# Kernel optimization log

Hardware: AMD Instinct MI355X
Metric: run time of the kernel (lower is better)

## Reference

```python
import jax, jax.numpy as jnp
import numpy as np

GRID = 192          # grid_size (scaled up from the module's toy 32)
H = 0.1             # cell_size
VISC = 0.01         # viscosity
DT = 0.01           # config.time_step, passed as forward's dt
GRAV = 9.81


def setup_inputs() -> dict:
    key = jax.random.key(0)
    velocity_field = jax.random.normal(key, (3, GRID, GRID, GRID), dtype=jnp.float32)
    return {"velocity_field": velocity_field}


def _nb_sum(f):
    # 6-neighbor sum on the interior of the last three axes
    return (f[..., 2:, 1:-1, 1:-1] + f[..., :-2, 1:-1, 1:-1]
            + f[..., 1:-1, 2:, 1:-1] + f[..., 1:-1, :-2, 1:-1]
            + f[..., 1:-1, 1:-1, 2:] + f[..., 1:-1, 1:-1, :-2])


def _fluid_step(vel):
    N = GRID
    dt = DT
    # --- add_gravity ---
    vel = vel.at[2].add(-GRAV * dt)
    # --- advect: semi-Lagrangian backtrace + trilinear interpolation ---
    coords = jnp.arange(N, dtype=vel.dtype)
    X, Y, Z = jnp.meshgrid(coords, coords, coords, indexing='ij')
    pos = jnp.stack([X, Y, Z]) - vel * (dt / H)        # [3,N,N,N] backtraced positions
    pos = jnp.clip(pos, 0.0, float(N - 2))
    i0 = jnp.floor(pos).astype(jnp.int32)              # base corner, i1 = i0+1 <= N-1
    w1 = pos - i0.astype(vel.dtype)
    w0 = 1.0 - w1
    ix, iy, iz = i0[0], i0[1], i0[2]
    wx0, wy0, wz0 = w0[0], w0[1], w0[2]
    wx1, wy1, wz1 = w1[0], w1[1], w1[2]

    def g(di, dj, dk):
        return vel[:, ix + di, iy + dj, iz + dk]        # gather -> [3,N,N,N]

    vel = (g(0, 0, 0) * wx0 * wy0 * wz0 + g(0, 0, 1) * wx0 * wy0 * wz1
           + g(0, 1, 0) * wx0 * wy1 * wz0 + g(0, 1, 1) * wx0 * wy1 * wz1
           + g(1, 0, 0) * wx1 * wy0 * wz0 + g(1, 0, 1) * wx1 * wy0 * wz1
           + g(1, 1, 0) * wx1 * wy1 * wz0 + g(1, 1, 1) * wx1 * wy1 * wz1)
    # --- diffuse: 5 Jacobi sweeps on the interior ---
    alpha = VISC * dt / (H * H)
    inv = 1.0 / (1.0 + 6.0 * alpha)
    for _ in range(5):
        interior = (vel[:, 1:-1, 1:-1, 1:-1] + alpha * _nb_sum(vel)) * inv
        vel = vel.at[:, 1:-1, 1:-1, 1:-1].set(interior)
    # --- project: central-difference divergence, 20 Jacobi pressure sweeps, gradient subtract ---
    div = jnp.zeros((N, N, N), vel.dtype)
    div_int = ((vel[0, 2:, 1:-1, 1:-1] - vel[0, :-2, 1:-1, 1:-1])
               + (vel[1, 1:-1, 2:, 1:-1] - vel[1, 1:-1, :-2, 1:-1])
               + (vel[2, 1:-1, 1:-1, 2:] - vel[2, 1:-1, 1:-1, :-2])) / (2.0 * H)
    div = div.at[1:-1, 1:-1, 1:-1].set(div_int)
    p = jnp.zeros_like(div)
    for _ in range(20):
        p = p.at[1:-1, 1:-1, 1:-1].set((div[1:-1, 1:-1, 1:-1] + _nb_sum(p)) / 6.0)
    inv2h = 1.0 / (2.0 * H)
    vel = vel.at[0, 1:-1, 1:-1, 1:-1].add(-(p[2:, 1:-1, 1:-1] - p[:-2, 1:-1, 1:-1]) * inv2h)
    vel = vel.at[1, 1:-1, 1:-1, 1:-1].add(-(p[1:-1, 2:, 1:-1] - p[1:-1, :-2, 1:-1]) * inv2h)
    vel = vel.at[2, 1:-1, 1:-1, 1:-1].add(-(p[1:-1, 1:-1, 2:] - p[1:-1, 1:-1, :-2]) * inv2h)
    return vel


def reference(velocity_field):
    return _fluid_step(velocity_field)
```

## Files before the change

kernel.cpp:

```cpp
#include <hip/hip_runtime.h>


constexpr int   N      = 192;
constexpr int   N2     = N * N;
constexpr int   N3     = N * N * N;
constexpr float GDT    = 9.81f * 0.01f;
constexpr float SCL    = 0.01f / 0.1f;
constexpr float ALPHA  = 0.01f * 0.01f / (0.1f * 0.1f);
constexpr float INVDIF = 1.0f / (1.0f + 6.0f * ALPHA);
constexpr float INV2H  = 1.0f / (2.0f * 0.1f);
constexpr float SIXTH  = 1.0f / 6.0f;

constexpr int NT4 = (N3 / 4) / 256;
constexpr int SLAB = NT4 / 8;

__device__ __forceinline__ int swz(int b) {
    return (b & 7) * SLAB + (b >> 3);
}

__device__ __forceinline__ void decomp(int id, int& i, int& j, int& k0) {
    i = id / N2;
    const int r = id - i * N2;
    j = r / N;
    k0 = r - j * N;
}

__global__ __launch_bounds__(192) void k_advect(const float* __restrict__ vin,
                                                float* __restrict__ vout) {
    const int k   = threadIdx.x;
    const int lin = blockIdx.y * 192 + blockIdx.x;
    const int x   = lin & 7;
    const int q   = lin >> 3;
    const int il  = q % 24;
    const int j   = q / 24;
    const int i   = x * 24 + il;
    const int id  = (i * N + j) * N + k;

    const float vx = vin[id];
    const float vy = vin[id + N3];
    const float vz = vin[id + 2 * N3] - GDT;

    float px = (float)i - vx * SCL;
    float py = (float)j - vy * SCL;
    float pz = (float)k - vz * SCL;
    const float hi = (float)(N - 2);
    px = fminf(fmaxf(px, 0.0f), hi);
    py = fminf(fmaxf(py, 0.0f), hi);
    pz = fminf(fmaxf(pz, 0.0f), hi);

    const int ix = (int)px;
    const int iy = (int)py;
    const int iz = (int)pz;
    const int base = (ix * N + iy) * N + iz;

    float g[3][8];
#pragma unroll
    for (int c = 0; c < 3; ++c) {
        const float* f = vin + c * N3 + base;
        g[c][0] = f[0];      g[c][1] = f[1];
        g[c][2] = f[N];      g[c][3] = f[N + 1];
        g[c][4] = f[N2];     g[c][5] = f[N2 + 1];
        g[c][6] = f[N2 + N]; g[c][7] = f[N2 + N + 1];
    }

    const float wx1 = px - (float)ix, wy1 = py - (float)iy, wz1 = pz - (float)iz;
    const float wx0 = 1.0f - wx1,     wy0 = 1.0f - wy1,     wz0 = 1.0f - wz1;
    const float w000 = wx0 * wy0 * wz0;
    const float w001 = wx0 * wy0 * wz1;
    const float w010 = wx0 * wy1 * wz0;
    const float w011 = wx0 * wy1 * wz1;
    const float w100 = wx1 * wy0 * wz0;
    const float w101 = wx1 * wy0 * wz1;
    const float w110 = wx1 * wy1 * wz0;
    const float w111 = wx1 * wy1 * wz1;

#pragma unroll
    for (int c = 0; c < 3; ++c) {
        float r = g[c][0] * w000 + g[c][1] * w001
                + g[c][2] * w010 + g[c][3] * w011
                + g[c][4] * w100 + g[c][5] * w101
                + g[c][6] * w110 + g[c][7] * w111;
        if (c == 2) r -= GDT;
        vout[c * N3 + id] = r;
    }
}

__global__ __launch_bounds__(256) void k_diffuse4(const float* __restrict__ vin,
                                                  float* __restrict__ vout) {
    const int gtid = swz(blockIdx.x) * 256 + threadIdx.x;
    const int id   = gtid << 2;
    int i, j, k0; decomp(id, i, j, k0);
    const int b = blockIdx.y * N3 + id;

    const float4 c = *(const float4*)(vin + b);
    float4 out = c;
    if (i != 0 && i != N - 1 && j != 0 && j != N - 1) {
        const float4 ip = *(const float4*)(vin + b + N2);
        const float4 im = *(const float4*)(vin + b - N2);
        const float4 jp = *(const float4*)(vin + b + N);
        const float4 jm = *(const float4*)(vin + b - N);
        const float  km = (k0 > 0)     ? vin[b - 1] : 0.0f;
        const float  kp = (k0 < N - 4) ? vin[b + 4] : 0.0f;
        out.x = (c.x + ALPHA * (im.x + ip.x + jm.x + jp.x + km  + c.y)) * INVDIF;
        out.y = (c.y + ALPHA * (im.y + ip.y + jm.y + jp.y + c.x + c.z)) * INVDIF;
        out.z = (c.z + ALPHA * (im.z + ip.z + jm.z + jp.z + c.y + c.w)) * INVDIF;
        out.w = (c.w + ALPHA * (im.w + ip.w + jm.w + jp.w + c.z + kp )) * INVDIF;
        if (k0 == 0)     out.x = c.x;
        if (k0 == N - 4) out.w = c.w;
    }
    *(float4*)(vout + b) = out;
}

__global__ __launch_bounds__(256) void k_div4(const float* __restrict__ v,
                                              float* __restrict__ dv) {
    const int gtid = swz(blockIdx.x) * 256 + threadIdx.x;
    const int id   = gtid << 2;
    int i, j, k0; decomp(id, i, j, k0);

    float4 out = make_float4(0.f, 0.f, 0.f, 0.f);
    if (i != 0 && i != N - 1 && j != 0 && j != N - 1) {
        const float4 xp = *(const float4*)(v + id + N2);
        const float4 xm = *(const float4*)(v + id - N2);
        const float4 yp = *(const float4*)(v + N3 + id + N);
        const float4 ym = *(const float4*)(v + N3 + id - N);
        const float4 z  = *(const float4*)(v + 2 * N3 + id);
        const float  zm = (k0 > 0)     ? v[2 * N3 + id - 1] : 0.0f;
        const float  zp = (k0 < N - 4) ? v[2 * N3 + id + 4] : 0.0f;
        out.x = ((xp.x - xm.x) + (yp.x - ym.x) + (z.y - zm )) * INV2H;
        out.y = ((xp.y - xm.y) + (yp.y - ym.y) + (z.z - z.x)) * INV2H;
        out.z = ((xp.z - xm.z) + (yp.z - ym.z) + (z.w - z.y)) * INV2H;
        out.w = ((xp.w - xm.w) + (yp.w - ym.w) + (zp  - z.z)) * INV2H;
        if (k0 == 0)     out.x = 0.f;
        if (k0 == N - 4) out.w = 0.f;
    }
    *(float4*)(dv + id) = out;
}

__global__ __launch_bounds__(256) void k_p2_4(const float* __restrict__ dv,
                                              float* __restrict__ p) {
    const int gtid = swz(blockIdx.x) * 256 + threadIdx.x;
    const int id   = gtid << 2;
    int i, j, k0; decomp(id, i, j, k0);

    float4 out = make_float4(0.f, 0.f, 0.f, 0.f);
    if (i != 0 && i != N - 1 && j != 0 && j != N - 1) {
        const float4 c  = *(const float4*)(dv + id);
        const float4 ip = *(const float4*)(dv + id + N2);
        const float4 im = *(const float4*)(dv + id - N2);
        const float4 jp = *(const float4*)(dv + id + N);
        const float4 jm = *(const float4*)(dv + id - N);
        const float  km = (k0 > 0)     ? dv[id - 1] : 0.0f;
        const float  kp = (k0 < N - 4) ? dv[id + 4] : 0.0f;
        out.x = (c.x + (im.x + ip.x + jm.x + jp.x + km  + c.y) * SIXTH) * SIXTH;
        out.y = (c.y + (im.y + ip.y + jm.y + jp.y + c.x + c.z) * SIXTH) * SIXTH;
        out.z = (c.z + (im.z + ip.z + jm.z + jp.z + c.y + c.w) * SIXTH) * SIXTH;
        out.w = (c.w + (im.w + ip.w + jm.w + jp.w + c.z + kp ) * SIXTH) * SIXTH;
        if (k0 == 0)     out.x = 0.f;
        if (k0 == N - 4) out.w = 0.f;
    }
    *(float4*)(p + id) = out;
}

__global__ __launch_bounds__(256) void k_jacobi4(const float* __restrict__ pin,
                                                 const float* __restrict__ dv,
                                                 float* __restrict__ pout) {
    const int gtid = swz(blockIdx.x) * 256 + threadIdx.x;
    const int id   = gtid << 2;
    int i, j, k0; decomp(id, i, j, k0);

    float4 out = make_float4(0.f, 0.f, 0.f, 0.f);
    if (i != 0 && i != N - 1 && j != 0 && j != N - 1) {
        const float4 c  = *(const float4*)(pin + id);
        const float4 ip = *(const float4*)(pin + id + N2);
        const float4 im = *(const float4*)(pin + id - N2);
        const float4 jp = *(const float4*)(pin + id + N);
        const float4 jm = *(const float4*)(pin + id - N);
        const float4 d  = *(const float4*)(dv + id);
        const float  km = (k0 > 0)     ? pin[id - 1] : 0.0f;
        const float  kp = (k0 < N - 4) ? pin[id + 4] : 0.0f;
        out.x = (d.x + im.x + ip.x + jm.x + jp.x + km  + c.y) * SIXTH;
        out.y = (d.y + im.y + ip.y + jm.y + jp.y + c.x + c.z) * SIXTH;
        out.z = (d.z + im.z + ip.z + jm.z + jp.z + c.y + c.w) * SIXTH;
        out.w = (d.w + im.w + ip.w + jm.w + jp.w + c.z + kp ) * SIXTH;
        if (k0 == 0)     out.x = 0.f;
        if (k0 == N - 4) out.w = 0.f;
    }
    *(float4*)(pout + id) = out;
}

__global__ __launch_bounds__(256) void k_grad4(float* __restrict__ vel,
                                               const float* __restrict__ p) {
    const int gtid = swz(blockIdx.x) * 256 + threadIdx.x;
    const int id   = gtid << 2;
    int i, j, k0; decomp(id, i, j, k0);
    if (i == 0 || i == N - 1 || j == 0 || j == N - 1) return;

    const float4 xp = *(const float4*)(p + id + N2);
    const float4 xm = *(const float4*)(p + id - N2);
    const float4 yp = *(const float4*)(p + id + N);
    const float4 ym = *(const float4*)(p + id - N);
    const float4 c  = *(const float4*)(p + id);
    const float  pm = (k0 > 0)     ? p[id - 1] : 0.0f;
    const float  pp = (k0 < N - 4) ? p[id + 4] : 0.0f;

    const bool bx = (k0 == 0);
    const bool bw = (k0 == N - 4);

    float4 v0 = *(float4*)(vel + id);
    if (!bx) v0.x -= (xp.x - xm.x) * INV2H;
             v0.y -= (xp.y - xm.y) * INV2H;
             v0.z -= (xp.z - xm.z) * INV2H;
    if (!bw) v0.w -= (xp.w - xm.w) * INV2H;
    *(float4*)(vel + id) = v0;

    float4 v1 = *(float4*)(vel + N3 + id);
    if (!bx) v1.x -= (yp.x - ym.x) * INV2H;
             v1.y -= (yp.y - ym.y) * INV2H;
             v1.z -= (yp.z - ym.z) * INV2H;
    if (!bw) v1.w -= (yp.w - ym.w) * INV2H;
    *(float4*)(vel + N3 + id) = v1;

    float4 v2 = *(float4*)(vel + 2 * N3 + id);
    if (!bx) v2.x -= (c.y - pm ) * INV2H;
             v2.y -= (c.z - c.x) * INV2H;
             v2.z -= (c.w - c.y) * INV2H;
    if (!bw) v2.w -= (pp  - c.z) * INV2H;
    *(float4*)(vel + 2 * N3 + id) = v2;
}

extern "C" void kernel_launch(void* const* d_in, const int* in_sizes, int n_in,
                              void* d_out, int out_size, void* d_ws, size_t ws_size,
                              hipStream_t stream) {
    const float* vin  = (const float*)d_in[0];
    float*       vout = (float*)d_out;
    float*       ws   = (float*)d_ws;

    float* velB = ws;
    float* dv   = ws;
    float* pA   = ws + N3;
    float* pB   = ws + 2 * N3;

    const dim3 blk(N, 1, 1);
    const dim3 grid1(N, N, 1);
    const dim3 blk4(256, 1, 1);
    const dim3 grid4_1(NT4, 1, 1);
    const dim3 grid4_3(NT4, 3, 1);

    k_advect<<<grid1, blk, 0, stream>>>(vin, velB);

    k_diffuse4<<<grid4_3, blk4, 0, stream>>>(velB, vout);
    k_diffuse4<<<grid4_3, blk4, 0, stream>>>(vout, velB);
    k_diffuse4<<<grid4_3, blk4, 0, stream>>>(velB, vout);
    k_diffuse4<<<grid4_3, blk4, 0, stream>>>(vout, velB);
    k_diffuse4<<<grid4_3, blk4, 0, stream>>>(velB, vout);

    k_div4<<<grid4_1, blk4, 0, stream>>>(vout, dv);
    k_p2_4<<<grid4_1, blk4, 0, stream>>>(dv, pA);
    float* pin  = pA;
    float* pout = pB;
    for (int s = 0; s < 18; ++s) {
        k_jacobi4<<<grid4_1, blk4, 0, stream>>>(pin, dv, pout);
        float* t = pin; pin = pout; pout = t;
    }
    k_grad4<<<grid4_1, blk4, 0, stream>>>(vout, pin);
}
```

Measured before the change: 644.6 us.

## Store pressure and divergence in fp16 and stage advect neighbourhood in LDS

```diff
diff --git a/kernel.cpp b/kernel.cpp
--- a/kernel.cpp
+++ b/kernel.cpp
@@ -1,4 +1,5 @@
 #include <hip/hip_runtime.h>
+#include <hip/hip_fp16.h>
 
 
 constexpr int   N      = 192;
@@ -25,8 +26,24 @@
     k0 = r - j * N;
 }
 
+union H4u { ushort4 u; __half h[4]; };
+__device__ __forceinline__ float4 ldh4(const __half* p) {
+    H4u t; t.u = *(const ushort4*)p;
+    return make_float4(__half2float(t.h[0]), __half2float(t.h[1]),
+                       __half2float(t.h[2]), __half2float(t.h[3]));
+}
+__device__ __forceinline__ void sth4(__half* p, float x, float y, float z, float w) {
+    H4u t;
+    t.h[0] = __float2half(x); t.h[1] = __float2half(y);
+    t.h[2] = __float2half(z); t.h[3] = __float2half(w);
+    *(ushort4*)p = t.u;
+}
+__device__ __forceinline__ float ldh(const __half* p) { return __half2float(*p); }
+
 __global__ __launch_bounds__(192) void k_advect(const float* __restrict__ vin,
                                                 float* __restrict__ vout) {
+    __shared__ float s[27 * 192];
+
     const int k   = threadIdx.x;
     const int lin = blockIdx.y * 192 + blockIdx.x;
     const int x   = lin & 7;
@@ -36,9 +53,29 @@
     const int i   = x * 24 + il;
     const int id  = (i * N + j) * N + k;
 
-    const float vx = vin[id];
-    const float vy = vin[id + N3];
-    const float vz = vin[id + 2 * N3] - GDT;
+    {
+        const int rsub = threadIdx.x / 48;
+        const int col  = (threadIdx.x - rsub * 48) * 4;
+#pragma unroll
+        for (int p = 0; p < 7; ++p) {
+            const int r = p * 4 + rsub;
+            if (r < 27) {
+                const int c   = r / 9;
+                const int rem = r - c * 9;
+                const int di  = rem / 3;
+                const int dj  = rem - di * 3;
+                const int gi  = min(max(i + di - 1, 0), N - 1);
+                const int gj  = min(max(j + dj - 1, 0), N - 1);
+                *(float4*)&s[r * 192 + col] =
+                    *(const float4*)&vin[c * N3 + gi * N2 + gj * N + col];
+            }
+        }
+    }
+    __syncthreads();
+
+    const float vx = s[4 * 192 + k];
+    const float vy = s[13 * 192 + k];
+    const float vz = s[22 * 192 + k] - GDT;
 
     float px = (float)i - vx * SCL;
     float py = (float)j - vy * SCL;
@@ -51,16 +88,33 @@
     const int ix = (int)px;
     const int iy = (int)py;
     const int iz = (int)pz;
-    const int base = (ix * N + iy) * N + iz;
 
     float g[3][8];
+    const bool in = (ix >= i - 1) & (ix <= i) & (iy >= j - 1) & (iy <= j);
+    if (in) {
+        const int li = ix - i + 1;
+        const int lj = iy - j + 1;
 #pragma unroll
-    for (int c = 0; c < 3; ++c) {
-        const float* f = vin + c * N3 + base;
-        g[c][0] = f[0];      g[c][1] = f[1];
-        g[c][2] = f[N];      g[c][3] = f[N + 1];
-        g[c][4] = f[N2];     g[c][5] = f[N2 + 1];
-        g[c][6] = f[N2 + N]; g[c][7] = f[N2 + N + 1];
+        for (int c = 0; c < 3; ++c) {
+            const int r00 = ((c * 3 + li) * 3 + lj) * 192 + iz;
+            const int r01 = r00 + 192;
+            const int r10 = r00 + 3 * 192;
+            const int r11 = r10 + 192;
+            g[c][0] = s[r00];     g[c][1] = s[r00 + 1];
+            g[c][2] = s[r01];     g[c][3] = s[r01 + 1];
+            g[c][4] = s[r10];     g[c][5] = s[r10 + 1];
+            g[c][6] = s[r11];     g[c][7] = s[r11 + 1];
+        }
+    } else {
+        const int base = (ix * N + iy) * N + iz;
+#pragma unroll
+        for (int c = 0; c < 3; ++c) {
+            const float* f = vin + c * N3 + base;
+            g[c][0] = f[0];      g[c][1] = f[1];
+            g[c][2] = f[N];      g[c][3] = f[N + 1];
+            g[c][4] = f[N2];     g[c][5] = f[N2 + 1];
+            g[c][6] = f[N2 + N]; g[c][7] = f[N2 + N + 1];
+        }
     }
 
     const float wx1 = px - (float)ix, wy1 = py - (float)iy, wz1 = pz - (float)iz;
@@ -112,12 +166,12 @@
 }
 
 __global__ __launch_bounds__(256) void k_div4(const float* __restrict__ v,
-                                              float* __restrict__ dv) {
-    const int gtid = swz(blockIdx.x) * 256 + threadIdx.x;
-    const int id   = gtid << 2;
-    int i, j, k0; decomp(id, i, j, k0);
-
-    float4 out = make_float4(0.f, 0.f, 0.f, 0.f);
+                                              __half* __restrict__ dv) {
+    const int gtid = swz(blockIdx.x) * 256 + threadIdx.x;
+    const int id   = gtid << 2;
+    int i, j, k0; decomp(id, i, j, k0);
+
+    float ox = 0.f, oy = 0.f, oz = 0.f, ow = 0.f;
     if (i != 0 && i != N - 1 && j != 0 && j != N - 1) {
         const float4 xp = *(const float4*)(v + id + N2);
         const float4 xm = *(const float4*)(v + id - N2);
@@ -126,82 +180,82 @@
         const float4 z  = *(const float4*)(v + 2 * N3 + id);
         const float  zm = (k0 > 0)     ? v[2 * N3 + id - 1] : 0.0f;
         const float  zp = (k0 < N - 4) ? v[2 * N3 + id + 4] : 0.0f;
-        out.x = ((xp.x - xm.x) + (yp.x - ym.x) + (z.y - zm )) * INV2H;
-        out.y = ((xp.y - xm.y) + (yp.y - ym.y) + (z.z - z.x)) * INV2H;
-        out.z = ((xp.z - xm.z) + (yp.z - ym.z) + (z.w - z.y)) * INV2H;
-        out.w = ((xp.w - xm.w) + (yp.w - ym.w) + (zp  - z.z)) * INV2H;
-        if (k0 == 0)     out.x = 0.f;
-        if (k0 == N - 4) out.w = 0.f;
-    }
-    *(float4*)(dv + id) = out;
-}
-
-__global__ __launch_bounds__(256) void k_p2_4(const float* __restrict__ dv,
-                                              float* __restrict__ p) {
-    const int gtid = swz(blockIdx.x) * 256 + threadIdx.x;
-    const int id   = gtid << 2;
-    int i, j, k0; decomp(id, i, j, k0);
-
-    float4 out = make_float4(0.f, 0.f, 0.f, 0.f);
+        ox = ((xp.x - xm.x) + (yp.x - ym.x) + (z.y - zm )) * INV2H;
+        oy = ((xp.y - xm.y) + (yp.y - ym.y) + (z.z - z.x)) * INV2H;
+        oz = ((xp.z - xm.z) + (yp.z - ym.z) + (z.w - z.y)) * INV2H;
+        ow = ((xp.w - xm.w) + (yp.w - ym.w) + (zp  - z.z)) * INV2H;
+        if (k0 == 0)     ox = 0.f;
+        if (k0 == N - 4) ow = 0.f;
+    }
+    sth4(dv + id, ox, oy, oz, ow);
+}
+
+__global__ __launch_bounds__(256) void k_p2_4(const __half* __restrict__ dv,
+                                              __half* __restrict__ p) {
+    const int gtid = swz(blockIdx.x) * 256 + threadIdx.x;
+    const int id   = gtid << 2;
+    int i, j, k0; decomp(id, i, j, k0);
+
+    float ox = 0.f, oy = 0.f, oz = 0.f, ow = 0.f;
     if (i != 0 && i != N - 1 && j != 0 && j != N - 1) {
-        const float4 c  = *(const float4*)(dv + id);
-        const float4 ip = *(const float4*)(dv + id + N2);
-        const float4 im = *(const float4*)(dv + id - N2);
-        const float4 jp = *(const float4*)(dv + id + N);
-        const float4 jm = *(const float4*)(dv + id - N);
-        const float  km = (k0 > 0)     ? dv[id - 1] : 0.0f;
-        const float  kp = (k0 < N - 4) ? dv[id + 4] : 0.0f;
-        out.x = (c.x + (im.x + ip.x + jm.x + jp.x + km  + c.y) * SIXTH) * SIXTH;
-        out.y = (c.y + (im.y + ip.y + jm.y + jp.y + c.x + c.z) * SIXTH) * SIXTH;
-        out.z = (c.z + (im.z + ip.z + jm.z + jp.z + c.y + c.w) * SIXTH) * SIXTH;
-        out.w = (c.w + (im.w + ip.w + jm.w + jp.w + c.z + kp ) * SIXTH) * SIXTH;
-        if (k0 == 0)     out.x = 0.f;
-        if (k0 == N - 4) out.w = 0.f;
-    }
-    *(float4*)(p + id) = out;
-}
-
-__global__ __launch_bounds__(256) void k_jacobi4(const float* __restrict__ pin,
-                                                 const float* __restrict__ dv,
-                                                 float* __restrict__ pout) {
-    const int gtid = swz(blockIdx.x) * 256 + threadIdx.x;
-    const int id   = gtid << 2;
-    int i, j, k0; decomp(id, i, j, k0);
-
-    float4 out = make_float4(0.f, 0.f, 0.f, 0.f);
+        const float4 c  = ldh4(dv + id);
+        const float4 ip = ldh4(dv + id + N2);
+        const float4 im = ldh4(dv + id - N2);
+        const float4 jp = ldh4(dv + id + N);
+        const float4 jm = ldh4(dv + id - N);
+        const float  km = (k0 > 0)     ? ldh(dv + id - 1) : 0.0f;
+        const float  kp = (k0 < N - 4) ? ldh(dv + id + 4) : 0.0f;
+        ox = (c.x + (im.x + ip.x + jm.x + jp.x + km  + c.y) * SIXTH) * SIXTH;
+        oy = (c.y + (im.y + ip.y + jm.y + jp.y + c.x + c.z) * SIXTH) * SIXTH;
+        oz = (c.z + (im.z + ip.z + jm.z + jp.z + c.y + c.w) * SIXTH) * SIXTH;
+        ow = (c.w + (im.w + ip.w + jm.w + jp.w + c.z + kp ) * SIXTH) * SIXTH;
+        if (k0 == 0)     ox = 0.f;
+        if (k0 == N - 4) ow = 0.f;
+    }
+    sth4(p + id, ox, oy, oz, ow);
+}
+
+__global__ __launch_bounds__(256) void k_jacobi4(const __half* __restrict__ pin,
+                                                 const __half* __restrict__ dv,
+                                                 __half* __restrict__ pout) {
+    const int gtid = swz(blockIdx.x) * 256 + threadIdx.x;
+    const int id   = gtid << 2;
+    int i, j, k0; decomp(id, i, j, k0);
+
+    float ox = 0.f, oy = 0.f, oz = 0.f, ow = 0.f;
     if (i != 0 && i != N - 1 && j != 0 && j != N - 1) {
-        const float4 c  = *(const float4*)(pin + id);
-        const float4 ip = *(const float4*)(pin + id + N2);
-        const float4 im = *(const float4*)(pin + id - N2);
-        const float4 jp = *(const float4*)(pin + id + N);
-        const float4 jm = *(const float4*)(pin + id - N);
-        const float4 d  = *(const float4*)(dv + id);
-        const float  km = (k0 > 0)     ? pin[id - 1] : 0.0f;
-        const float  kp = (k0 < N - 4) ? pin[id + 4] : 0.0f;
-        out.x = (d.x + im.x + ip.x + jm.x + jp.x + km  + c.y) * SIXTH;
-        out.y = (d.y + im.y + ip.y + jm.y + jp.y + c.x + c.z) * SIXTH;
-        out.z = (d.z + im.z + ip.z + jm.z + jp.z + c.y + c.w) * SIXTH;
-        out.w = (d.w + im.w + ip.w + jm.w + jp.w + c.z + kp ) * SIXTH;
-        if (k0 == 0)     out.x = 0.f;
-        if (k0 == N - 4) out.w = 0.f;
-    }
-    *(float4*)(pout + id) = out;
+        const float4 c  = ldh4(pin + id);
+        const float4 ip = ldh4(pin + id + N2);
+        const float4 im = ldh4(pin + id - N2);
+        const float4 jp = ldh4(pin + id + N);
+        const float4 jm = ldh4(pin + id - N);
+        const float4 d  = ldh4(dv + id);
+        const float  km = (k0 > 0)     ? ldh(pin + id - 1) : 0.0f;
+        const float  kp = (k0 < N - 4) ? ldh(pin + id + 4) : 0.0f;
+        ox = (d.x + im.x + ip.x + jm.x + jp.x + km  + c.y) * SIXTH;
+        oy = (d.y + im.y + ip.y + jm.y + jp.y + c.x + c.z) * SIXTH;
+        oz = (d.z + im.z + ip.z + jm.z + jp.z + c.y + c.w) * SIXTH;
+        ow = (d.w + im.w + ip.w + jm.w + jp.w + c.z + kp ) * SIXTH;
+        if (k0 == 0)     ox = 0.f;
+        if (k0 == N - 4) ow = 0.f;
+    }
+    sth4(pout + id, ox, oy, oz, ow);
 }
 
 __global__ __launch_bounds__(256) void k_grad4(float* __restrict__ vel,
-                                               const float* __restrict__ p) {
+                                               const __half* __restrict__ p) {
     const int gtid = swz(blockIdx.x) * 256 + threadIdx.x;
     const int id   = gtid << 2;
     int i, j, k0; decomp(id, i, j, k0);
     if (i == 0 || i == N - 1 || j == 0 || j == N - 1) return;
 
-    const float4 xp = *(const float4*)(p + id + N2);
-    const float4 xm = *(const float4*)(p + id - N2);
-    const float4 yp = *(const float4*)(p + id + N);
-    const float4 ym = *(const float4*)(p + id - N);
-    const float4 c  = *(const float4*)(p + id);
-    const float  pm = (k0 > 0)     ? p[id - 1] : 0.0f;
-    const float  pp = (k0 < N - 4) ? p[id + 4] : 0.0f;
+    const float4 xp = ldh4(p + id + N2);
+    const float4 xm = ldh4(p + id - N2);
+    const float4 yp = ldh4(p + id + N);
+    const float4 ym = ldh4(p + id - N);
+    const float4 c  = ldh4(p + id);
+    const float  pm = (k0 > 0)     ? ldh(p + id - 1) : 0.0f;
+    const float  pp = (k0 < N - 4) ? ldh(p + id + 4) : 0.0f;
 
     const bool bx = (k0 == 0);
     const bool bw = (k0 == N - 4);
@@ -235,10 +289,11 @@
     float*       vout = (float*)d_out;
     float*       ws   = (float*)d_ws;
 
-    float* velB = ws;
-    float* dv   = ws;
-    float* pA   = ws + N3;
-    float* pB   = ws + 2 * N3;
+    float*  velB = ws;
+    __half* hws  = (__half*)d_ws;
+    __half* dv   = hws;
+    __half* pA   = hws + N3;
+    __half* pB   = hws + 2 * N3;
 
     const dim3 blk(N, 1, 1);
     const dim3 grid1(N, N, 1);
@@ -256,11 +311,11 @@
 
     k_div4<<<grid4_1, blk4, 0, stream>>>(vout, dv);
     k_p2_4<<<grid4_1, blk4, 0, stream>>>(dv, pA);
-    float* pin  = pA;
-    float* pout = pB;
+    __half* pin  = pA;
+    __half* pout = pB;
     for (int s = 0; s < 18; ++s) {
         k_jacobi4<<<grid4_1, blk4, 0, stream>>>(pin, dv, pout);
-        float* t = pin; pin = pout; pout = t;
+        __half* t = pin; pin = pout; pout = t;
     }
     k_grad4<<<grid4_1, blk4, 0, stream>>>(vout, pin);
 }
```

New measurement: 573.6 us. 1.12x faster.
